# Optimization experiments

Hardware: AMD Instinct MI355X
Metric: run time of the kernel (lower is better)

## Reference

```python
import jax, jax.numpy as jnp
import numpy as np

N_SEQ, L_RES, Q_STATES = 8192, 256, 21


def setup_inputs() -> dict:
    key = jax.random.key(0)
    k_x, k_h, k_j, k_perm = jax.random.split(key, 4)
    # One-hot encoded MSA: [N, L, q]
    aa_idx = jax.random.randint(k_x, (N_SEQ, L_RES), 0, Q_STATES)
    X = jax.nn.one_hot(aa_idx, Q_STATES, dtype=jnp.float32)
    # Model parameters (torch.randn init in the original module)
    h = jax.random.normal(k_h, (L_RES, Q_STATES), dtype=jnp.float32)
    J = jax.random.normal(k_j, (L_RES, Q_STATES, L_RES, Q_STATES), dtype=jnp.float32)
    # Order of residues to update during the Gibbs sweep (a permutation of 0..L-1)
    residue_idxs = jax.random.permutation(k_perm, L_RES)
    return {"X": X, "residue_idxs": residue_idxs, "h": h, "J": J, "beta": 1.0}


def reference(X, residue_idxs, h, J, beta):
    """One sequential Gibbs sweep over the residues (plmDCA.forward).

    For each residue i (in the given order):
      logits_i = h[i] + X_flat @ J[i].reshape(q, L*q).T   (equiv. einsum below)
      X[:, i]  = one_hot(sample ~ softmax(beta * logits_i))
    The loop is a true data-dependent recurrence -> lax.scan.
    """
    n, l, q = X.shape
    n_steps = residue_idxs.shape[0]
    keys = jax.random.split(jax.random.key(42), n_steps)

    def step(X_cur, inp):
        i, k = inp
        J_i = jnp.take(J, i, axis=0)  # [q, L, q]
        h_i = jnp.take(h, i, axis=0)  # [q]
        # [N, q] cavity logits for residue i
        logits = h_i + jnp.einsum('nlb,alb->na', X_cur, J_i)
        # multinomial over softmax(beta * logits) == categorical(beta * logits)
        s = jax.random.categorical(k, beta * logits, axis=-1)  # [N]
        X_cur = X_cur.at[:, i, :].set(jax.nn.one_hot(s, q, dtype=X_cur.dtype))
        return X_cur, None

    X_out, _ = jax.lax.scan(step, X, (residue_idxs, keys))
    return X_out
```

## Files before the change

### kernel.cpp

```cpp
#include <hip/hip_runtime.h>
#include <stdint.h>
#include <math.h>


#define NSEQ 8192
#define LRES 256
#define QST  21
#define SPB  32
#define NTHREADS (SPB * QST)

struct KcTbl {
  unsigned char thr[LRES];
  constexpr KcTbl() : thr() {
    for (int i = 0; i < LRES; ++i) thr[i] = 255;
    for (int m = 1; m < 19; ++m) {
      int l = (288 * m) / 21;
      thr[l] = (unsigned char)(288 * m - 21 * l);
    }
  }
};
static constexpr KcTbl KC_TBL{};

__device__ __forceinline__ uint32_t rotl32(uint32_t v, uint32_t r) {
  return (v << r) | (v >> (32u - r));
}

__device__ __forceinline__ void threefry2x32(uint32_t k0, uint32_t k1,
                                             uint32_t c0, uint32_t c1,
                                             uint32_t& o0, uint32_t& o1) {
  uint32_t ks2 = k0 ^ k1 ^ 0x1BD11BDAu;
  uint32_t x0 = c0 + k0;
  uint32_t x1 = c1 + k1;
#define TF_ROUND(r) { x0 += x1; x1 = rotl32(x1, r); x1 ^= x0; }
  TF_ROUND(13u) TF_ROUND(15u) TF_ROUND(26u) TF_ROUND(6u)
  x0 += k1;  x1 += ks2 + 1u;
  TF_ROUND(17u) TF_ROUND(29u) TF_ROUND(16u) TF_ROUND(24u)
  x0 += ks2; x1 += k0 + 2u;
  TF_ROUND(13u) TF_ROUND(15u) TF_ROUND(26u) TF_ROUND(6u)
  x0 += k0;  x1 += k1 + 3u;
  TF_ROUND(17u) TF_ROUND(29u) TF_ROUND(16u) TF_ROUND(24u)
  x0 += k1;  x1 += ks2 + 4u;
  TF_ROUND(13u) TF_ROUND(15u) TF_ROUND(26u) TF_ROUND(6u)
  x0 += ks2; x1 += k0 + 5u;
#undef TF_ROUND
  o0 = x0; o1 = x1;
}

__device__ __forceinline__ float gumbel_f32(uint32_t bits) {
  float f = __uint_as_float((bits >> 9) | 0x3f800000u) - 1.0f;
  float u = fmaxf(1.17549435e-38f, f + 1.17549435e-38f);
  float w = (float)log((double)u);
  float t = -w;
  float g = -(float)log((double)t);
  return g;
}

__global__ __launch_bounds__(NTHREADS)
void gibbs_sweep(const float* __restrict__ X, const int* __restrict__ order,
                 const float* __restrict__ h, const float* __restrict__ J,
                 const float* __restrict__ betaPtr, float* __restrict__ out) {
  __shared__ uint32_t sbst[(LRES / 4) * SPB];
  __shared__ float    vals[QST][SPB];
  __shared__ uint32_t tk0[LRES], tk1[LRES];

  const int nl  = threadIdx.x;
  const int a   = threadIdx.y;
  const int tid = nl + SPB * a;
  const int n0  = blockIdx.x * SPB;
  const int n   = n0 + nl;
  const float beta = betaPtr[0];

  for (int t = tid; t < LRES; t += NTHREADS) {
    uint32_t o0, o1;
    threefry2x32(0u, 42u, 0u, (uint32_t)t, o0, o1);
    tk0[t] = o0; tk1[t] = o1;
  }

  for (int idx = tid; idx < (LRES / 4) * SPB; idx += NTHREADS) {
    int s  = idx & (SPB - 1);
    int wg = idx / SPB;
    uint32_t w = 0;
#pragma unroll
    for (int j = 0; j < 4; ++j) {
      int l = 4 * wg + j;
      const float* xp = X + ((size_t)(n0 + s) * LRES + l) * QST;
      int b = 0;
#pragma unroll
      for (int q = 0; q < QST; ++q) b = (xp[q] > 0.5f) ? q : b;
      w |= ((uint32_t)b) << (8 * j);
    }
    sbst[wg * SPB + s] = w;
  }
  __syncthreads();

  for (int t = 0; t < LRES; ++t) {
    const int i = order[t];
    const uint32_t rowoff = (uint32_t)(i * QST + a) * (uint32_t)(LRES * QST);

    float tot = 0.0f, part = 0.0f;
#pragma unroll
    for (int lg = 0; lg < LRES / 4; ++lg) {
      uint32_t w = sbst[lg * SPB + nl];
#pragma unroll
      for (int j = 0; j < 4; ++j) {
        const int l = 4 * lg + j;
        uint32_t b = (w >> (8 * j)) & 0xffu;
        float jv = J[rowoff + (uint32_t)(l * QST) + b];
        const int thr = KC_TBL.thr[l];
        if (thr == 255) {
          part += jv;
        } else if (thr == 0) {
          tot += part; part = jv;
        } else {
          if ((int)b >= thr) { tot += part; part = jv; }
          else               { part += jv; tot += part; part = 0.0f; }
        }
      }
    }
    tot += part;

    float lo = h[i * QST + a] + tot;

    uint32_t o0, o1;
    threefry2x32(tk0[t], tk1[t], 0u, (uint32_t)(n * QST + a), o0, o1);
    float g = gumbel_f32(o0 ^ o1);

    vals[a][nl] = g + beta * lo;
    __syncthreads();

    if (a == 0) {
      float best = vals[0][nl];
      int bi = 0;
#pragma unroll
      for (int q = 1; q < QST; ++q) {
        float vv = vals[q][nl];
        if (vv > best) { best = vv; bi = q; }
      }
      unsigned char* bp = reinterpret_cast<unsigned char*>(sbst);
      bp[((i >> 2) * SPB + nl) * 4 + (i & 3)] = (unsigned char)bi;
    }
    __syncthreads();
  }

  const size_t base = (size_t)n0 * LRES * QST;
  for (int idx = tid; idx < SPB * LRES * QST; idx += NTHREADS) {
    int s   = idx / (LRES * QST);
    int rem = idx - s * (LRES * QST);
    int l   = rem / QST;
    int q   = rem - l * QST;
    uint32_t w = sbst[(l >> 2) * SPB + s];
    int b = (int)((w >> (8 * (l & 3))) & 0xffu);
    out[base + idx] = (b == q) ? 1.0f : 0.0f;
  }
}

extern "C" void kernel_launch(void* const* d_in, const int* in_sizes, int n_in,
                              void* d_out, int out_size, void* d_ws, size_t ws_size,
                              hipStream_t stream) {
  const float* X     = (const float*)d_in[0];
  const int*   order = (const int*)  d_in[1];
  const float* h     = (const float*)d_in[2];
  const float* J     = (const float*)d_in[3];
  const float* beta  = (const float*)d_in[4];
  float* out = (float*)d_out;

  dim3 grid(NSEQ / SPB);
  dim3 block(SPB, QST);
  hipLaunchKernelGGL(gibbs_sweep, grid, block, 0, stream, X, order, h, J, beta, out);
}
```

Measured before the change: 5.908 ms.

## Stage J rows through double-buffered LDS chunks with cooperative float4 loads

Each residue's J row slice (21 strips by 256x21 floats) is now loaded in chunks of 32 residues into a double-buffered shared-memory buffer with coalesced float4 loads, prefetching the next chunk (or the next residue's first chunk) while the current one is consumed. The per-thread gather then reads from LDS instead of issuing scattered global loads. The residue order is also cached in LDS. This adds a __syncthreads per chunk and large LDS usage that limits occupancy to one block per CU.

After: 17.75 ms. 200% more time.

```diff
diff --git a/kernel.cpp b/kernel.cpp
--- a/kernel.cpp
+++ b/kernel.cpp
@@ -8,6 +8,14 @@
 #define QST  21
 #define SPB  32
 #define NTHREADS (SPB * QST)
+#define CH   32
+#define NCH  (LRES / CH)
+#define STRIPW 688
+#define BUFW (QST * STRIPW)
+#define CHU4 168
+#define UNITS (QST * CHU4)
+#define STRIPU4 1344
+#define ROWU4 28224
 
 struct KcTbl {
   unsigned char thr[LRES];
@@ -55,13 +63,15 @@
   return g;
 }
 
-__global__ __launch_bounds__(NTHREADS)
+__global__ __launch_bounds__(NTHREADS, 1)
 void gibbs_sweep(const float* __restrict__ X, const int* __restrict__ order,
                  const float* __restrict__ h, const float* __restrict__ J,
                  const float* __restrict__ betaPtr, float* __restrict__ out) {
+  __shared__ __align__(16) float jchunk[2][BUFW];
   __shared__ uint32_t sbst[(LRES / 4) * SPB];
   __shared__ float    vals[QST][SPB];
   __shared__ uint32_t tk0[LRES], tk1[LRES];
+  __shared__ int      sord[LRES];
 
   const int nl  = threadIdx.x;
   const int a   = threadIdx.y;
@@ -74,6 +84,7 @@
     uint32_t o0, o1;
     threefry2x32(0u, 42u, 0u, (uint32_t)t, o0, o1);
     tk0[t] = o0; tk1[t] = o1;
+    sord[t] = order[t];
   }
 
   for (int idx = tid; idx < (LRES / 4) * SPB; idx += NTHREADS) {
@@ -93,29 +104,70 @@
   }
   __syncthreads();
 
+  const float4* Jv = (const float4*)J;
+
+  {
+    const size_t rb = (size_t)sord[0] * ROWU4;
+#pragma unroll
+    for (int k = 0; k < 6; ++k) {
+      int u = tid + NTHREADS * k;
+      if (u < UNITS) {
+        int aa = u / CHU4;
+        int ww = u - aa * CHU4;
+        float4 v = Jv[rb + (size_t)(aa * STRIPU4 + ww)];
+        *(float4*)&jchunk[0][aa * STRIPW + 4 * ww] = v;
+      }
+    }
+  }
+  __syncthreads();
+
+  const float* gbA = &jchunk[0][0] + a * STRIPW;
+  const float* gbB = &jchunk[1][0] + a * STRIPW;
+
   for (int t = 0; t < LRES; ++t) {
-    const int i = order[t];
-    const uint32_t rowoff = (uint32_t)(i * QST + a) * (uint32_t)(LRES * QST);
+    const int i = sord[t];
 
     float tot = 0.0f, part = 0.0f;
 #pragma unroll
-    for (int lg = 0; lg < LRES / 4; ++lg) {
-      uint32_t w = sbst[lg * SPB + nl];
-#pragma unroll
-      for (int j = 0; j < 4; ++j) {
-        const int l = 4 * lg + j;
-        uint32_t b = (w >> (8 * j)) & 0xffu;
-        float jv = J[rowoff + (uint32_t)(l * QST) + b];
-        const int thr = KC_TBL.thr[l];
-        if (thr == 255) {
-          part += jv;
-        } else if (thr == 0) {
-          tot += part; part = jv;
-        } else {
-          if ((int)b >= thr) { tot += part; part = jv; }
-          else               { part += jv; tot += part; part = 0.0f; }
+    for (int c = 0; c < NCH; ++c) {
+      {
+        const int nrow = (c < NCH - 1) ? i : sord[(t + 1) & (LRES - 1)];
+        const int ncc  = (c < NCH - 1) ? c + 1 : 0;
+        const size_t rb = (size_t)nrow * ROWU4 + (size_t)(ncc * CHU4);
+        float* dst = &jchunk[(c + 1) & 1][0];
+#pragma unroll
+        for (int k = 0; k < 6; ++k) {
+          int u = tid + NTHREADS * k;
+          if (u < UNITS) {
+            int aa = u / CHU4;
+            int ww = u - aa * CHU4;
+            float4 v = Jv[rb + (size_t)(aa * STRIPU4 + ww)];
+            *(float4*)(dst + (aa * STRIPW + 4 * ww)) = v;
+          }
         }
       }
+
+      const float* gb = (c & 1) ? gbB : gbA;
+#pragma unroll
+      for (int lg = 0; lg < CH / 4; ++lg) {
+        uint32_t w = sbst[(c * (CH / 4) + lg) * SPB + nl];
+#pragma unroll
+        for (int j = 0; j < 4; ++j) {
+          const int l = c * CH + 4 * lg + j;
+          uint32_t b = (w >> (8 * j)) & 0xffu;
+          float jv = gb[(4 * lg + j) * QST + b];
+          const int thr = KC_TBL.thr[l];
+          if (thr == 255) {
+            part += jv;
+          } else if (thr == 0) {
+            tot += part; part = jv;
+          } else {
+            if ((int)b >= thr) { tot += part; part = jv; }
+            else               { part += jv; tot += part; part = 0.0f; }
+          }
+        }
+      }
+      __syncthreads();
     }
     tot += part;
 
```

## Transpose J into a padded [i][l][b][a] workspace layout for coalesced gathers

Applied to the files above, without the earlier changes.

Adds a pre-pass kernel that rewrites J into a per-residue layout with the output state a innermost, padded to 22. The sweep kernel swaps thread roles so the 21 state threads of one sequence read adjacent addresses, loading float2 pairs instead of scattered gathers strided by L*q. It also caches the residue order in shared memory. The cost is an extra full read and write of J (about 22/21 of its size) on every call, plus a dependence on workspace size, with the old kernel kept as a fallback.

Result: slower. 22.74 ms (+285.0%).

```diff
diff --git a/kernel.cpp b/kernel.cpp
--- a/kernel.cpp
+++ b/kernel.cpp
@@ -6,8 +6,12 @@
 #define NSEQ 8192
 #define LRES 256
 #define QST  21
+#define APAD 22
 #define SPB  32
 #define NTHREADS (SPB * QST)
+#define ROWT (LRES * QST * APAD)
+#define ROWJ (QST * LRES * QST)
+#define WS_NEED ((size_t)LRES * ROWT * sizeof(float))
 
 struct KcTbl {
   unsigned char thr[LRES];
@@ -56,9 +60,131 @@
 }
 
 __global__ __launch_bounds__(NTHREADS)
-void gibbs_sweep(const float* __restrict__ X, const int* __restrict__ order,
-                 const float* __restrict__ h, const float* __restrict__ J,
-                 const float* __restrict__ betaPtr, float* __restrict__ out) {
+void transpose_J(const float* __restrict__ J, float* __restrict__ JT) {
+  const int i = blockIdx.x;
+  const float* src = J + (size_t)i * ROWJ;
+  float* dst = JT + (size_t)i * ROWT;
+  for (int o = threadIdx.x; o < ROWT; o += NTHREADS) {
+    int a    = o % APAD;
+    int rest = o / APAD;
+    float v = 0.0f;
+    if (a < QST) {
+      int b = rest % QST;
+      int l = rest / QST;
+      v = src[((size_t)a * LRES + l) * QST + b];
+    }
+    dst[o] = v;
+  }
+}
+
+__global__ __launch_bounds__(NTHREADS, 1)
+void gibbs_sweep_T(const float* __restrict__ X, const int* __restrict__ order,
+                   const float* __restrict__ h, const float* __restrict__ JT,
+                   const float* __restrict__ betaPtr, float* __restrict__ out) {
+  __shared__ uint32_t sbst[(LRES / 4) * SPB];
+  __shared__ float    vals[SPB][QST];
+  __shared__ uint32_t tk0[LRES], tk1[LRES];
+  __shared__ int      sord[LRES];
+
+  const int a   = threadIdx.x;
+  const int nl  = threadIdx.y;
+  const int tid = a + QST * nl;
+  const int n0  = blockIdx.x * SPB;
+  const int n   = n0 + nl;
+  const float beta = betaPtr[0];
+
+  for (int t = tid; t < LRES; t += NTHREADS) {
+    uint32_t o0, o1;
+    threefry2x32(0u, 42u, 0u, (uint32_t)t, o0, o1);
+    tk0[t] = o0; tk1[t] = o1;
+    sord[t] = order[t];
+  }
+
+  for (int idx = tid; idx < (LRES / 4) * SPB; idx += NTHREADS) {
+    int s  = idx & (SPB - 1);
+    int wg = idx / SPB;
+    uint32_t w = 0;
+#pragma unroll
+    for (int j = 0; j < 4; ++j) {
+      int l = 4 * wg + j;
+      const float* xp = X + ((size_t)(n0 + s) * LRES + l) * QST;
+      int b = 0;
+#pragma unroll
+      for (int q = 0; q < QST; ++q) b = (xp[q] > 0.5f) ? q : b;
+      w |= ((uint32_t)b) << (8 * j);
+    }
+    sbst[wg * SPB + s] = w;
+  }
+  __syncthreads();
+
+  const bool odd = (a & 1);
+
+  for (int t = 0; t < LRES; ++t) {
+    const int i = sord[t];
+    const float* rp = JT + (size_t)i * ROWT + (uint32_t)(a & ~1);
+
+    float tot = 0.0f, part = 0.0f;
+#pragma unroll
+    for (int lg = 0; lg < LRES / 4; ++lg) {
+      uint32_t w = sbst[lg * SPB + nl];
+#pragma unroll
+      for (int j = 0; j < 4; ++j) {
+        const int l = 4 * lg + j;
+        uint32_t b = (w >> (8 * j)) & 0xffu;
+        float2 v = *(const float2*)(rp + (uint32_t)(l * QST + b) * APAD);
+        float jv = odd ? v.y : v.x;
+        const int thr = KC_TBL.thr[l];
+        if (thr == 255) {
+          part += jv;
+        } else if (thr == 0) {
+          tot += part; part = jv;
+        } else {
+          if ((int)b >= thr) { tot += part; part = jv; }
+          else               { part += jv; tot += part; part = 0.0f; }
+        }
+      }
+    }
+    tot += part;
+
+    float lo = h[i * QST + a] + tot;
+
+    uint32_t o0, o1;
+    threefry2x32(tk0[t], tk1[t], 0u, (uint32_t)(n * QST + a), o0, o1);
+    float g = gumbel_f32(o0 ^ o1);
+
+    vals[nl][a] = g + beta * lo;
+    __syncthreads();
+
+    if (a == 0) {
+      float best = vals[nl][0];
+      int bi = 0;
+#pragma unroll
+      for (int q = 1; q < QST; ++q) {
+        float vv = vals[nl][q];
+        if (vv > best) { best = vv; bi = q; }
+      }
+      unsigned char* bp = reinterpret_cast<unsigned char*>(sbst);
+      bp[((i >> 2) * SPB + nl) * 4 + (i & 3)] = (unsigned char)bi;
+    }
+    __syncthreads();
+  }
+
+  const size_t base = (size_t)n0 * LRES * QST;
+  for (int idx = tid; idx < SPB * LRES * QST; idx += NTHREADS) {
+    int s   = idx / (LRES * QST);
+    int rem = idx - s * (LRES * QST);
+    int l   = rem / QST;
+    int q   = rem - l * QST;
+    uint32_t w = sbst[(l >> 2) * SPB + s];
+    int b = (int)((w >> (8 * (l & 3))) & 0xffu);
+    out[base + idx] = (b == q) ? 1.0f : 0.0f;
+  }
+}
+
+__global__ __launch_bounds__(NTHREADS)
+void gibbs_sweep_fb(const float* __restrict__ X, const int* __restrict__ order,
+                    const float* __restrict__ h, const float* __restrict__ J,
+                    const float* __restrict__ betaPtr, float* __restrict__ out) {
   __shared__ uint32_t sbst[(LRES / 4) * SPB];
   __shared__ float    vals[QST][SPB];
   __shared__ uint32_t tk0[LRES], tk1[LRES];
@@ -75,7 +201,6 @@
     threefry2x32(0u, 42u, 0u, (uint32_t)t, o0, o1);
     tk0[t] = o0; tk1[t] = o1;
   }
-
   for (int idx = tid; idx < (LRES / 4) * SPB; idx += NTHREADS) {
     int s  = idx & (SPB - 1);
     int wg = idx / SPB;
@@ -96,7 +221,6 @@
   for (int t = 0; t < LRES; ++t) {
     const int i = order[t];
     const uint32_t rowoff = (uint32_t)(i * QST + a) * (uint32_t)(LRES * QST);
-
     float tot = 0.0f, part = 0.0f;
 #pragma unroll
     for (int lg = 0; lg < LRES / 4; ++lg) {
@@ -118,16 +242,12 @@
       }
     }
     tot += part;
-
     float lo = h[i * QST + a] + tot;
-
     uint32_t o0, o1;
     threefry2x32(tk0[t], tk1[t], 0u, (uint32_t)(n * QST + a), o0, o1);
     float g = gumbel_f32(o0 ^ o1);
-
     vals[a][nl] = g + beta * lo;
     __syncthreads();
-
     if (a == 0) {
       float best = vals[0][nl];
       int bi = 0;
@@ -164,7 +284,13 @@
   const float* beta  = (const float*)d_in[4];
   float* out = (float*)d_out;
 
-  dim3 grid(NSEQ / SPB);
-  dim3 block(SPB, QST);
-  hipLaunchKernelGGL(gibbs_sweep, grid, block, 0, stream, X, order, h, J, beta, out);
-}
+  if (ws_size >= WS_NEED) {
+    float* JT = (float*)d_ws;
+    hipLaunchKernelGGL(transpose_J, dim3(LRES), dim3(NTHREADS), 0, stream, J, JT);
+    hipLaunchKernelGGL(gibbs_sweep_T, dim3(NSEQ / SPB), dim3(QST, SPB), 0, stream,
+                       X, order, h, JT, beta, out);
+  } else {
+    hipLaunchKernelGGL(gibbs_sweep_fb, dim3(NSEQ / SPB), dim3(SPB, QST), 0, stream,
+                       X, order, h, J, beta, out);
+  }
+}
```
